# Performance work log

Measured on AMD Instinct MI355X. Metric: run time of the kernel, lower is better.

## Reference

```python
import math
import jax, jax.numpy as jnp
import numpy as np

B, L, H, E = 4, 2048, 16, 64
D = 64

def setup_inputs() -> dict:
    key = jax.random.key(0)
    kq, kk, kv = jax.random.split(key, 3)
    queries = jax.random.normal(kq, (B, L, H, E), dtype=jnp.float32)
    keys = jax.random.normal(kk, (B, L, H, E), dtype=jnp.float32)
    values = jax.random.normal(kv, (B, L, H, D), dtype=jnp.float32)
    return {"queries": queries, "keys": keys, "values": values}

def reference(queries, keys, values):
    # queries [B,L,H,E], keys [B,S,H,E], values [B,S,H,D]; causal => L==S
    Bq, Lq, Hq, Eq = queries.shape
    scale = 1.0 / math.sqrt(Eq)
    # scores [B,H,L,S]
    scores = jnp.einsum('blhe,bshe->bhls', queries, keys)
    S = keys.shape[1]
    causal = jnp.triu(jnp.ones((Lq, S), dtype=bool), k=1)  # True above diagonal
    scores = jnp.where(causal[None, None, :, :], -jnp.inf, scores)
    A = jax.nn.softmax(scale * scores, axis=-1)  # dropout_rate=0.0 (eval)
    V = jnp.einsum('bhls,bshd->blhd', A, values)
    return (V, A)
```

## Files before the change

### kernel.cpp

```cpp
#include <hip/hip_runtime.h>

#define B_ 4
#define L_ 2048
#define H_ 16
#define E_ 64
#define D_ 64
#define S_ 2048
#define LDP 72

typedef __bf16 bf16x8 __attribute__((ext_vector_type(8)));
typedef __bf16 bf16x4 __attribute__((ext_vector_type(4)));
typedef float  f32x4  __attribute__((ext_vector_type(4)));

__global__ __launch_bounds__(256) void convert_qk(
    const float* __restrict__ Q, const float* __restrict__ K,
    __bf16* __restrict__ Qb, __bf16* __restrict__ Kb)
{
    const int g = blockIdx.x * 256 + threadIdx.x;
    const float* src = blockIdx.y ? K : Q;
    __bf16* dst = blockIdx.y ? Kb : Qb;
    const int e4 = g & 15;
    const int h  = (g >> 4) & (H_ - 1);
    const int l  = (g >> 8) & (L_ - 1);
    const int b  = g >> 19;
    f32x4 v = *(const f32x4*)(src + (size_t)g * 4);
    bf16x4 o;
    o[0] = (__bf16)v[0]; o[1] = (__bf16)v[1];
    o[2] = (__bf16)v[2]; o[3] = (__bf16)v[3];
    *(bf16x4*)(dst + (((size_t)(b * H_ + h) * L_ + l) * E_ + e4 * 4)) = o;
}

__global__ __launch_bounds__(256) void convert_vt(
    const float* __restrict__ V, __bf16* __restrict__ Vt)
{
    __shared__ __bf16 T[64 * 68];
    const int tid = threadIdx.x;
    const int lt  = blockIdx.x & 31;
    const int bh  = blockIdx.x >> 5;
    const int b = bh >> 4, h = bh & 15;
    const int l0 = lt * 64;
    for (int i = 0; i < 4; ++i) {
        const int lr = (tid >> 4) + 16 * i;
        const int c4 = (tid & 15) * 4;
        f32x4 v = *(const f32x4*)(V + ((size_t)(b * L_ + l0 + lr) * H_ + h) * D_ + c4);
        bf16x4 o;
        o[0] = (__bf16)v[0]; o[1] = (__bf16)v[1];
        o[2] = (__bf16)v[2]; o[3] = (__bf16)v[3];
        *(bf16x4*)&T[lr * 68 + c4] = o;
    }
    __syncthreads();
    for (int i = 0; i < 4; ++i) {
        const int d  = (tid >> 4) + 16 * i;
        const int s4 = (tid & 15) * 4;
        bf16x4 o;
        o[0] = T[(s4 + 0) * 68 + d];
        o[1] = T[(s4 + 1) * 68 + d];
        o[2] = T[(s4 + 2) * 68 + d];
        o[3] = T[(s4 + 3) * 68 + d];
        *(bf16x4*)(Vt + ((size_t)bh * 64 + d) * L_ + l0 + s4) = o;
    }
}

__global__ __launch_bounds__(256) void fullattn_kernel(
    const __bf16* __restrict__ Qb, const __bf16* __restrict__ Kb,
    const __bf16* __restrict__ Vt, float* __restrict__ Vout,
    float* __restrict__ Aout)
{
    __shared__ __bf16 P_lds[64 * LDP];

    const int tid  = threadIdx.x;
    const int wave = tid >> 6;
    const int lane = tid & 63;
    const int ln15 = lane & 15;
    const int quad = lane >> 4;

    const int bh = blockIdx.x & 63;
    const int qt = 31 - (blockIdx.x >> 6);
    const int b  = bh >> 4;
    const int h  = bh & 15;
    const int q0 = qt * 64;
    const int nb = qt + 1;

    const float C1 = 0.125f * 1.44269504089f;
    const float C2 = -16.0f * 1.44269504089f;

    const __bf16* Qh = Qb + (size_t)bh * L_ * E_;
    const __bf16* Kh = Kb + (size_t)bh * L_ * E_;
    const __bf16* Vh = Vt + (size_t)bh * 64 * L_;

    bf16x8 qfrag[2];
    {
        const __bf16* qp = Qh + (size_t)(q0 + 16 * wave + ln15) * E_ + quad * 8;
        qfrag[0] = *(const bf16x8*)(qp);
        qfrag[1] = *(const bf16x8*)(qp + 32);
    }

    float sums[4] = {0.f, 0.f, 0.f, 0.f};
    for (int kb = 0; kb < nb; ++kb) {
        const bool diag = (kb == qt);
        const __bf16* kp = Kh + (size_t)(kb * 64 + ln15) * E_ + quad * 8;
#pragma unroll
        for (int t = 0; t < 4; ++t) {
            const __bf16* kpt = kp + t * 16 * E_;
            f32x4 acc = {0.f, 0.f, 0.f, 0.f};
            acc = __builtin_amdgcn_mfma_f32_16x16x32_bf16(qfrag[0], *(const bf16x8*)(kpt), acc, 0, 0, 0);
            acc = __builtin_amdgcn_mfma_f32_16x16x32_bf16(qfrag[1], *(const bf16x8*)(kpt + 32), acc, 0, 0, 0);
            const int scol = 16 * t + ln15;
#pragma unroll
            for (int r = 0; r < 4; ++r) {
                const int lrow = 16 * wave + quad * 4 + r;
                float p = (diag && (scol > lrow)) ? 0.0f
                        : __builtin_amdgcn_exp2f(fmaf(acc[r], C1, C2));
                sums[r] += p;
            }
        }
    }
    float rinv[4];
#pragma unroll
    for (int r = 0; r < 4; ++r) {
        float s = sums[r];
        s += __shfl_xor(s, 1);
        s += __shfl_xor(s, 2);
        s += __shfl_xor(s, 4);
        s += __shfl_xor(s, 8);
        rinv[r] = 1.0f / s;
    }

    f32x4 oacc[4] = {{0.f,0.f,0.f,0.f},{0.f,0.f,0.f,0.f},
                     {0.f,0.f,0.f,0.f},{0.f,0.f,0.f,0.f}};
    const size_t arow0 = (size_t)bh * L_ + q0;

    for (int kb = 0; kb < nb; ++kb) {
        const bool diag = (kb == qt);
        const __bf16* kp = Kh + (size_t)(kb * 64 + ln15) * E_ + quad * 8;
#pragma unroll
        for (int t = 0; t < 4; ++t) {
            const __bf16* kpt = kp + t * 16 * E_;
            f32x4 acc = {0.f, 0.f, 0.f, 0.f};
            acc = __builtin_amdgcn_mfma_f32_16x16x32_bf16(qfrag[0], *(const bf16x8*)(kpt), acc, 0, 0, 0);
            acc = __builtin_amdgcn_mfma_f32_16x16x32_bf16(qfrag[1], *(const bf16x8*)(kpt + 32), acc, 0, 0, 0);
            const int scol = 16 * t + ln15;
#pragma unroll
            for (int r = 0; r < 4; ++r) {
                const int lrow = 16 * wave + quad * 4 + r;
                float p = (diag && (scol > lrow)) ? 0.0f
                        : __builtin_amdgcn_exp2f(fmaf(acc[r], C1, C2));
                const float a = p * rinv[r];
                Aout[(arow0 + lrow) * S_ + kb * 64 + scol] = a;
                P_lds[lrow * LDP + scol] = (__bf16)a;
            }
        }

        bf16x8 afr0 = *(const bf16x8*)&P_lds[(16 * wave + ln15) * LDP + quad * 8];
        bf16x8 afr1 = *(const bf16x8*)&P_lds[(16 * wave + ln15) * LDP + quad * 8 + 32];
        const __bf16* vp = Vh + (size_t)ln15 * L_ + kb * 64 + quad * 8;
#pragma unroll
        for (int t = 0; t < 4; ++t) {
            const __bf16* vpt = vp + (size_t)t * 16 * L_;
            oacc[t] = __builtin_amdgcn_mfma_f32_16x16x32_bf16(afr0, *(const bf16x8*)(vpt), oacc[t], 0, 0, 0);
            oacc[t] = __builtin_amdgcn_mfma_f32_16x16x32_bf16(afr1, *(const bf16x8*)(vpt + 32), oacc[t], 0, 0, 0);
        }
    }

    {
        const int c0 = nb * 64;
        const f32x4 z = {0.f, 0.f, 0.f, 0.f};
        for (int r = 0; r < 16; ++r) {
            float* ap = Aout + (arow0 + 16 * wave + r) * S_;
            for (int c = c0 + lane * 4; c < S_; c += 256)
                *(f32x4*)(ap + c) = z;
        }
    }

#pragma unroll
    for (int t = 0; t < 4; ++t)
#pragma unroll
        for (int r = 0; r < 4; ++r) {
            const int l = q0 + 16 * wave + quad * 4 + r;
            Vout[((size_t)(b * L_ + l) * H_ + h) * D_ + 16 * t + ln15] = oacc[t][r];
        }
}

extern "C" void kernel_launch(void* const* d_in, const int* in_sizes, int n_in,
                              void* d_out, int out_size, void* d_ws, size_t ws_size,
                              hipStream_t stream) {
    const float* Q = (const float*)d_in[0];
    const float* K = (const float*)d_in[1];
    const float* V = (const float*)d_in[2];
    float* Vout = (float*)d_out;
    float* Aout = Vout + (size_t)B_ * L_ * H_ * D_;

    __bf16* Qb = (__bf16*)d_ws;
    __bf16* Kb = Qb + (size_t)B_ * H_ * L_ * E_;
    __bf16* Vt = Kb + (size_t)B_ * H_ * L_ * E_;

    hipLaunchKernelGGL(convert_qk, dim3((B_ * L_ * H_ * E_) / (256 * 4), 2), dim3(256),
                       0, stream, Q, K, Qb, Kb);
    hipLaunchKernelGGL(convert_vt, dim3(B_ * H_ * (L_ / 64)), dim3(256),
                       0, stream, V, Vt);
    hipLaunchKernelGGL(fullattn_kernel, dim3(B_ * H_ * (L_ / 64)), dim3(256),
                       0, stream, Qb, Kb, Vt, Vout, Aout);
}
```

Measured before the change: 1.495 ms.

## Pre-swizzle Q/K/V into MFMA fragment layout and split attention into sums/out kernels

Conversion kernels now write Q, K and V in a fragment-major swizzled layout, so each lane's MFMA operand is one contiguous 16-byte load per 512-element chunk. Attention is split into a row-sum kernel that writes reciprocal sums to workspace and an output kernel that reads them. Both kernels register-prefetch the next K block (and the V block) and peel the diagonal block so off-diagonal blocks skip the mask check. Probability and output stores are made nontemporal. The split adds a kernel launch and a workspace round trip for the reciprocal sums, and the extra register buffers may lower occupancy.

```diff
diff --git a/kernel.cpp b/kernel.cpp
--- a/kernel.cpp
+++ b/kernel.cpp
@@ -12,110 +12,120 @@
 typedef __bf16 bf16x4 __attribute__((ext_vector_type(4)));
 typedef float  f32x4  __attribute__((ext_vector_type(4)));
 
-__global__ __launch_bounds__(256) void convert_qk(
+#define C1f (0.125f * 1.44269504089f)
+#define C2f (-16.0f * 1.44269504089f)
+
+__global__ __launch_bounds__(256) void convert_qk_sw(
     const float* __restrict__ Q, const float* __restrict__ K,
-    __bf16* __restrict__ Qb, __bf16* __restrict__ Kb)
+    __bf16* __restrict__ Qsw, __bf16* __restrict__ Ksw)
 {
     const int g = blockIdx.x * 256 + threadIdx.x;
     const float* src = blockIdx.y ? K : Q;
-    __bf16* dst = blockIdx.y ? Kb : Qb;
-    const int e4 = g & 15;
-    const int h  = (g >> 4) & (H_ - 1);
-    const int l  = (g >> 8) & (L_ - 1);
-    const int b  = g >> 19;
-    f32x4 v = *(const f32x4*)(src + (size_t)g * 4);
-    bf16x4 o;
-    o[0] = (__bf16)v[0]; o[1] = (__bf16)v[1];
-    o[2] = (__bf16)v[2]; o[3] = (__bf16)v[3];
-    *(bf16x4*)(dst + (((size_t)(b * H_ + h) * L_ + l) * E_ + e4 * 4)) = o;
-}
-
-__global__ __launch_bounds__(256) void convert_vt(
-    const float* __restrict__ V, __bf16* __restrict__ Vt)
+    __bf16* dst = blockIdx.y ? Ksw : Qsw;
+    const int l  = g & 63;
+    const int f  = (g >> 6) & 7;
+    const int tl = (g >> 9) & 31;
+    const int bh = g >> 14;
+    const int b = bh >> 4, h = bh & 15;
+    const int s  = tl * 64 + (f >> 1) * 16 + (l & 15);
+    const int e0 = (l >> 4) * 8 + (f & 1) * 32;
+    const float* sp = src + (((size_t)(b * L_ + s) * H_ + h) * E_ + e0);
+    f32x4 x = *(const f32x4*)sp;
+    f32x4 y = *(const f32x4*)(sp + 4);
+    bf16x8 o;
+    o[0]=(__bf16)x[0]; o[1]=(__bf16)x[1]; o[2]=(__bf16)x[2]; o[3]=(__bf16)x[3];
+    o[4]=(__bf16)y[0]; o[5]=(__bf16)y[1]; o[6]=(__bf16)y[2]; o[7]=(__bf16)y[3];
+    *(bf16x8*)(dst + (size_t)g * 8) = o;
+}
+
+__global__ __launch_bounds__(256) void convert_v_sw(
+    const float* __restrict__ V, __bf16* __restrict__ Vsw)
 {
     __shared__ __bf16 T[64 * 68];
     const int tid = threadIdx.x;
-    const int lt  = blockIdx.x & 31;
+    const int tl  = blockIdx.x & 31;
     const int bh  = blockIdx.x >> 5;
     const int b = bh >> 4, h = bh & 15;
-    const int l0 = lt * 64;
+    const int l0 = tl * 64;
     for (int i = 0; i < 4; ++i) {
         const int lr = (tid >> 4) + 16 * i;
         const int c4 = (tid & 15) * 4;
         f32x4 v = *(const f32x4*)(V + ((size_t)(b * L_ + l0 + lr) * H_ + h) * D_ + c4);
         bf16x4 o;
-        o[0] = (__bf16)v[0]; o[1] = (__bf16)v[1];
-        o[2] = (__bf16)v[2]; o[3] = (__bf16)v[3];
+        o[0]=(__bf16)v[0]; o[1]=(__bf16)v[1]; o[2]=(__bf16)v[2]; o[3]=(__bf16)v[3];
         *(bf16x4*)&T[lr * 68 + c4] = o;
     }
     __syncthreads();
-    for (int i = 0; i < 4; ++i) {
-        const int d  = (tid >> 4) + 16 * i;
-        const int s4 = (tid & 15) * 4;
-        bf16x4 o;
-        o[0] = T[(s4 + 0) * 68 + d];
-        o[1] = T[(s4 + 1) * 68 + d];
-        o[2] = T[(s4 + 2) * 68 + d];
-        o[3] = T[(s4 + 3) * 68 + d];
-        *(bf16x4*)(Vt + ((size_t)bh * 64 + d) * L_ + l0 + s4) = o;
-    }
-}
-
-__global__ __launch_bounds__(256) void fullattn_kernel(
-    const __bf16* __restrict__ Qb, const __bf16* __restrict__ Kb,
-    const __bf16* __restrict__ Vt, float* __restrict__ Vout,
-    float* __restrict__ Aout)
-{
-    __shared__ __bf16 P_lds[64 * LDP];
-
-    const int tid  = threadIdx.x;
-    const int wave = tid >> 6;
-    const int lane = tid & 63;
-    const int ln15 = lane & 15;
-    const int quad = lane >> 4;
-
+    for (int i = 0; i < 2; ++i) {
+        const int o = i * 256 + tid;
+        const int l = o & 63, f = (o >> 6) & 7;
+        const int d  = (f >> 1) * 16 + (l & 15);
+        const int s0 = (l >> 4) * 8 + (f & 1) * 32;
+        bf16x8 vv;
+#pragma unroll
+        for (int j = 0; j < 8; ++j) vv[j] = T[(s0 + j) * 68 + d];
+        *(bf16x8*)(Vsw + ((((size_t)bh * 32 + tl) * 8 + f) * 64 + l) * 8) = vv;
+    }
+}
+
+#define LOADF(dst, base) do {                                               \
+    const __bf16* _p0 = (base); const __bf16* _p1 = _p0 + 2048;             \
+    dst[0]=*(const bf16x8*)(_p0);      dst[1]=*(const bf16x8*)(_p0+512);    \
+    dst[2]=*(const bf16x8*)(_p0+1024); dst[3]=*(const bf16x8*)(_p0+1536);   \
+    dst[4]=*(const bf16x8*)(_p1);      dst[5]=*(const bf16x8*)(_p1+512);    \
+    dst[6]=*(const bf16x8*)(_p1+1024); dst[7]=*(const bf16x8*)(_p1+1536);   \
+} while (0)
+
+__global__ __launch_bounds__(256) void attn_sums(
+    const __bf16* __restrict__ Qsw, const __bf16* __restrict__ Ksw,
+    float* __restrict__ Rinv)
+{
+    const int tid = threadIdx.x, wave = tid >> 6, lane = tid & 63;
+    const int ln15 = lane & 15, quad = lane >> 4;
     const int bh = blockIdx.x & 63;
     const int qt = 31 - (blockIdx.x >> 6);
-    const int b  = bh >> 4;
-    const int h  = bh & 15;
-    const int q0 = qt * 64;
-    const int nb = qt + 1;
-
-    const float C1 = 0.125f * 1.44269504089f;
-    const float C2 = -16.0f * 1.44269504089f;
-
-    const __bf16* Qh = Qb + (size_t)bh * L_ * E_;
-    const __bf16* Kh = Kb + (size_t)bh * L_ * E_;
-    const __bf16* Vh = Vt + (size_t)bh * 64 * L_;
+    const size_t tileId = (size_t)bh * 32 + qt;
 
     bf16x8 qfrag[2];
     {
-        const __bf16* qp = Qh + (size_t)(q0 + 16 * wave + ln15) * E_ + quad * 8;
-        qfrag[0] = *(const bf16x8*)(qp);
-        qfrag[1] = *(const bf16x8*)(qp + 32);
-    }
-
+        const __bf16* qp = Qsw + (tileId * 8 + 2 * wave) * 512 + (size_t)lane * 8;
+        qfrag[0] = *(const bf16x8*)qp;
+        qfrag[1] = *(const bf16x8*)(qp + 512);
+    }
+    const __bf16* Kh = Ksw + (size_t)bh * 32 * 4096 + (size_t)lane * 8;
+
+    bf16x8 kf[8], kn[8];
+    LOADF(kf, Kh);
     float sums[4] = {0.f, 0.f, 0.f, 0.f};
-    for (int kb = 0; kb < nb; ++kb) {
-        const bool diag = (kb == qt);
-        const __bf16* kp = Kh + (size_t)(kb * 64 + ln15) * E_ + quad * 8;
-#pragma unroll
-        for (int t = 0; t < 4; ++t) {
-            const __bf16* kpt = kp + t * 16 * E_;
+    for (int kb = 0; kb < qt; ++kb) {
+        LOADF(kn, Kh + (size_t)(kb + 1) * 4096);
+#pragma unroll
+        for (int t = 0; t < 4; ++t) {
             f32x4 acc = {0.f, 0.f, 0.f, 0.f};
-            acc = __builtin_amdgcn_mfma_f32_16x16x32_bf16(qfrag[0], *(const bf16x8*)(kpt), acc, 0, 0, 0);
-            acc = __builtin_amdgcn_mfma_f32_16x16x32_bf16(qfrag[1], *(const bf16x8*)(kpt + 32), acc, 0, 0, 0);
-            const int scol = 16 * t + ln15;
-#pragma unroll
-            for (int r = 0; r < 4; ++r) {
-                const int lrow = 16 * wave + quad * 4 + r;
-                float p = (diag && (scol > lrow)) ? 0.0f
-                        : __builtin_amdgcn_exp2f(fmaf(acc[r], C1, C2));
-                sums[r] += p;
-            }
-        }
-    }
-    float rinv[4];
+            acc = __builtin_amdgcn_mfma_f32_16x16x32_bf16(qfrag[0], kf[2*t],   acc, 0, 0, 0);
+            acc = __builtin_amdgcn_mfma_f32_16x16x32_bf16(qfrag[1], kf[2*t+1], acc, 0, 0, 0);
+#pragma unroll
+            for (int r = 0; r < 4; ++r)
+                sums[r] += __builtin_amdgcn_exp2f(fmaf(acc[r], C1f, C2f));
+        }
+#pragma unroll
+        for (int i = 0; i < 8; ++i) kf[i] = kn[i];
+    }
+#pragma unroll
+    for (int t = 0; t < 4; ++t) {
+        f32x4 acc = {0.f, 0.f, 0.f, 0.f};
+        acc = __builtin_amdgcn_mfma_f32_16x16x32_bf16(qfrag[0], kf[2*t],   acc, 0, 0, 0);
+        acc = __builtin_amdgcn_mfma_f32_16x16x32_bf16(qfrag[1], kf[2*t+1], acc, 0, 0, 0);
+        const int scol = 16 * t + ln15;
+#pragma unroll
+        for (int r = 0; r < 4; ++r) {
+            const int lrow = 16 * wave + quad * 4 + r;
+            float p = (scol > lrow) ? 0.0f
+                    : __builtin_amdgcn_exp2f(fmaf(acc[r], C1f, C2f));
+            sums[r] += p;
+        }
+    }
+    float out[4];
 #pragma unroll
     for (int r = 0; r < 4; ++r) {
         float s = sums[r];
@@ -123,62 +133,129 @@
         s += __shfl_xor(s, 2);
         s += __shfl_xor(s, 4);
         s += __shfl_xor(s, 8);
-        rinv[r] = 1.0f / s;
-    }
+        out[r] = 1.0f / s;
+    }
+    if (ln15 == 0) {
+#pragma unroll
+        for (int r = 0; r < 4; ++r)
+            Rinv[tileId * 64 + 16 * wave + quad * 4 + r] = out[r];
+    }
+}
+
+__global__ __launch_bounds__(256) void attn_out(
+    const __bf16* __restrict__ Qsw, const __bf16* __restrict__ Ksw,
+    const __bf16* __restrict__ Vsw, const float* __restrict__ Rinv,
+    float* __restrict__ Vout, float* __restrict__ Aout)
+{
+    __shared__ __bf16 P_lds[64 * LDP];
+
+    const int tid = threadIdx.x, wave = tid >> 6, lane = tid & 63;
+    const int ln15 = lane & 15, quad = lane >> 4;
+    const int bh = blockIdx.x & 63;
+    const int qt = 31 - (blockIdx.x >> 6);
+    const int b = bh >> 4, h = bh & 15;
+    const int q0 = qt * 64;
+    const size_t tileId = (size_t)bh * 32 + qt;
+
+    bf16x8 qfrag[2];
+    {
+        const __bf16* qp = Qsw + (tileId * 8 + 2 * wave) * 512 + (size_t)lane * 8;
+        qfrag[0] = *(const bf16x8*)qp;
+        qfrag[1] = *(const bf16x8*)(qp + 512);
+    }
+    float rinv[4];
+#pragma unroll
+    for (int r = 0; r < 4; ++r)
+        rinv[r] = Rinv[tileId * 64 + 16 * wave + quad * 4 + r];
+
+    const __bf16* Kh = Ksw + (size_t)bh * 32 * 4096 + (size_t)lane * 8;
+    const __bf16* Vh = Vsw + (size_t)bh * 32 * 4096 + (size_t)lane * 8;
+
+    const size_t arow0 = (size_t)bh * L_ + q0;
+    float* ap[4];
+#pragma unroll
+    for (int r = 0; r < 4; ++r)
+        ap[r] = Aout + (arow0 + 16 * wave + quad * 4 + r) * S_ + ln15;
+
+    const int plw = (16 * wave + quad * 4) * LDP + ln15;
+    const int plr = (16 * wave + ln15) * LDP + quad * 8;
 
     f32x4 oacc[4] = {{0.f,0.f,0.f,0.f},{0.f,0.f,0.f,0.f},
                      {0.f,0.f,0.f,0.f},{0.f,0.f,0.f,0.f}};
-    const size_t arow0 = (size_t)bh * L_ + q0;
-
-    for (int kb = 0; kb < nb; ++kb) {
-        const bool diag = (kb == qt);
-        const __bf16* kp = Kh + (size_t)(kb * 64 + ln15) * E_ + quad * 8;
-#pragma unroll
-        for (int t = 0; t < 4; ++t) {
-            const __bf16* kpt = kp + t * 16 * E_;
+    bf16x8 kf[8], kn[8], vf[8];
+    LOADF(kf, Kh);
+
+    for (int kb = 0; kb < qt; ++kb) {
+        LOADF(vf, Vh + (size_t)kb * 4096);
+        LOADF(kn, Kh + (size_t)(kb + 1) * 4096);
+#pragma unroll
+        for (int t = 0; t < 4; ++t) {
             f32x4 acc = {0.f, 0.f, 0.f, 0.f};
-            acc = __builtin_amdgcn_mfma_f32_16x16x32_bf16(qfrag[0], *(const bf16x8*)(kpt), acc, 0, 0, 0);
-            acc = __builtin_amdgcn_mfma_f32_16x16x32_bf16(qfrag[1], *(const bf16x8*)(kpt + 32), acc, 0, 0, 0);
-            const int scol = 16 * t + ln15;
+            acc = __builtin_amdgcn_mfma_f32_16x16x32_bf16(qfrag[0], kf[2*t],   acc, 0, 0, 0);
+            acc = __builtin_amdgcn_mfma_f32_16x16x32_bf16(qfrag[1], kf[2*t+1], acc, 0, 0, 0);
 #pragma unroll
             for (int r = 0; r < 4; ++r) {
-                const int lrow = 16 * wave + quad * 4 + r;
-                float p = (diag && (scol > lrow)) ? 0.0f
-                        : __builtin_amdgcn_exp2f(fmaf(acc[r], C1, C2));
-                const float a = p * rinv[r];
-                Aout[(arow0 + lrow) * S_ + kb * 64 + scol] = a;
-                P_lds[lrow * LDP + scol] = (__bf16)a;
+                float a = __builtin_amdgcn_exp2f(fmaf(acc[r], C1f, C2f)) * rinv[r];
+                __builtin_nontemporal_store(a, ap[r] + 16 * t);
+                P_lds[plw + r * LDP + 16 * t] = (__bf16)a;
             }
         }
-
-        bf16x8 afr0 = *(const bf16x8*)&P_lds[(16 * wave + ln15) * LDP + quad * 8];
-        bf16x8 afr1 = *(const bf16x8*)&P_lds[(16 * wave + ln15) * LDP + quad * 8 + 32];
-        const __bf16* vp = Vh + (size_t)ln15 * L_ + kb * 64 + quad * 8;
-#pragma unroll
-        for (int t = 0; t < 4; ++t) {
-            const __bf16* vpt = vp + (size_t)t * 16 * L_;
-            oacc[t] = __builtin_amdgcn_mfma_f32_16x16x32_bf16(afr0, *(const bf16x8*)(vpt), oacc[t], 0, 0, 0);
-            oacc[t] = __builtin_amdgcn_mfma_f32_16x16x32_bf16(afr1, *(const bf16x8*)(vpt + 32), oacc[t], 0, 0, 0);
-        }
-    }
-
-    {
-        const int c0 = nb * 64;
+        bf16x8 afr0 = *(const bf16x8*)&P_lds[plr];
+        bf16x8 afr1 = *(const bf16x8*)&P_lds[plr + 32];
+#pragma unroll
+        for (int t = 0; t < 4; ++t) {
+            oacc[t] = __builtin_amdgcn_mfma_f32_16x16x32_bf16(afr0, vf[2*t],   oacc[t], 0, 0, 0);
+            oacc[t] = __builtin_amdgcn_mfma_f32_16x16x32_bf16(afr1, vf[2*t+1], oacc[t], 0, 0, 0);
+        }
+#pragma unroll
+        for (int i = 0; i < 8; ++i) kf[i] = kn[i];
+#pragma unroll
+        for (int r = 0; r < 4; ++r) ap[r] += 64;
+    }
+
+    LOADF(vf, Vh + (size_t)qt * 4096);
+#pragma unroll
+    for (int t = 0; t < 4; ++t) {
+        f32x4 acc = {0.f, 0.f, 0.f, 0.f};
+        acc = __builtin_amdgcn_mfma_f32_16x16x32_bf16(qfrag[0], kf[2*t],   acc, 0, 0, 0);
+        acc = __builtin_amdgcn_mfma_f32_16x16x32_bf16(qfrag[1], kf[2*t+1], acc, 0, 0, 0);
+        const int scol = 16 * t + ln15;
+#pragma unroll
+        for (int r = 0; r < 4; ++r) {
+            const int lrow = 16 * wave + quad * 4 + r;
+            float a = (scol > lrow) ? 0.0f
+                    : __builtin_amdgcn_exp2f(fmaf(acc[r], C1f, C2f)) * rinv[r];
+            __builtin_nontemporal_store(a, ap[r] + 16 * t);
+            P_lds[plw + r * LDP + 16 * t] = (__bf16)a;
+        }
+    }
+    {
+        bf16x8 afr0 = *(const bf16x8*)&P_lds[plr];
+        bf16x8 afr1 = *(const bf16x8*)&P_lds[plr + 32];
+#pragma unroll
+        for (int t = 0; t < 4; ++t) {
+            oacc[t] = __builtin_amdgcn_mfma_f32_16x16x32_bf16(afr0, vf[2*t],   oacc[t], 0, 0, 0);
+            oacc[t] = __builtin_amdgcn_mfma_f32_16x16x32_bf16(afr1, vf[2*t+1], oacc[t], 0, 0, 0);
+        }
+    }
+
+    {
+        const int c0 = (qt + 1) * 64;
         const f32x4 z = {0.f, 0.f, 0.f, 0.f};
         for (int r = 0; r < 16; ++r) {
-            float* ap = Aout + (arow0 + 16 * wave + r) * S_;
+            float* zp = Aout + (arow0 + 16 * wave + r) * S_;
             for (int c = c0 + lane * 4; c < S_; c += 256)
-                *(f32x4*)(ap + c) = z;
-        }
-    }
-
-#pragma unroll
-    for (int t = 0; t < 4; ++t)
-#pragma unroll
-        for (int r = 0; r < 4; ++r) {
-            const int l = q0 + 16 * wave + quad * 4 + r;
-            Vout[((size_t)(b * L_ + l) * H_ + h) * D_ + 16 * t + ln15] = oacc[t][r];
-        }
+                __builtin_nontemporal_store(z, (f32x4*)(zp + c));
+        }
+    }
+
+#pragma unroll
+    for (int r = 0; r < 4; ++r) {
+        float* vo = Vout + (((size_t)(b * L_ + q0 + 16 * wave + quad * 4 + r)) * H_ + h) * D_ + ln15;
+#pragma unroll
+        for (int t = 0; t < 4; ++t)
+            __builtin_nontemporal_store(oacc[t][r], vo + 16 * t);
+    }
 }
 
 extern "C" void kernel_launch(void* const* d_in, const int* in_sizes, int n_in,
@@ -190,14 +267,14 @@
     float* Vout = (float*)d_out;
     float* Aout = Vout + (size_t)B_ * L_ * H_ * D_;
 
-    __bf16* Qb = (__bf16*)d_ws;
-    __bf16* Kb = Qb + (size_t)B_ * H_ * L_ * E_;
-    __bf16* Vt = Kb + (size_t)B_ * H_ * L_ * E_;
-
-    hipLaunchKernelGGL(convert_qk, dim3((B_ * L_ * H_ * E_) / (256 * 4), 2), dim3(256),
-                       0, stream, Q, K, Qb, Kb);
-    hipLaunchKernelGGL(convert_vt, dim3(B_ * H_ * (L_ / 64)), dim3(256),
-                       0, stream, V, Vt);
-    hipLaunchKernelGGL(fullattn_kernel, dim3(B_ * H_ * (L_ / 64)), dim3(256),
-                       0, stream, Qb, Kb, Vt, Vout, Aout);
-}
+    __bf16* Qsw = (__bf16*)d_ws;
+    __bf16* Ksw = Qsw + (size_t)B_ * H_ * L_ * E_;
+    __bf16* Vsw = Ksw + (size_t)B_ * H_ * L_ * E_;
+    float*  Rinv = (float*)(Vsw + (size_t)B_ * H_ * L_ * D_);
+
+    hipLaunchKernelGGL(convert_qk_sw, dim3(4096, 2), dim3(256), 0, stream, Q, K, Qsw, Ksw);
+    hipLaunchKernelGGL(convert_v_sw, dim3(B_ * H_ * (L_ / 64)), dim3(256), 0, stream, V, Vsw);
+    hipLaunchKernelGGL(attn_sums, dim3(B_ * H_ * (L_ / 64)), dim3(256), 0, stream, Qsw, Ksw, Rinv);
+    hipLaunchKernelGGL(attn_out, dim3(B_ * H_ * (L_ / 64)), dim3(256), 0, stream,
+                       Qsw, Ksw, Vsw, Rinv, Vout, Aout);
+}
```

New measurement: 1.306 ms. 1.14x faster.
